# Performance work log

Hardware: AMD Instinct MI355X
Metric: run time of the kernel (lower is better)

## Reference

```python
import jax, jax.numpy as jnp
import numpy as np

WS = 8
SHIFT = 4


def _cpb_constants(ws):
    rc = np.arange(-(ws - 1), ws, dtype=np.float32)
    gh, gw = np.meshgrid(rc, rc, indexing='ij')
    table = np.stack([gh, gw], axis=-1)[None]  # (1, 2ws-1, 2ws-1, 2)
    table = table / (ws - 1) * 8.0
    table = np.sign(table) * np.log2(np.abs(table) + 1.0) / np.log2(8.0)
    c = np.arange(ws)
    ch, cw = np.meshgrid(c, c, indexing='ij')
    flat = np.stack([ch.ravel(), cw.ravel()])  # (2, N)
    rel = (flat[:, :, None] - flat[:, None, :]).transpose(1, 2, 0).copy()
    rel[..., 0] += ws - 1
    rel[..., 1] += ws - 1
    rel[..., 0] *= 2 * ws - 1
    rpi = rel.sum(-1)  # (N, N) int
    return table.astype(np.float32), rpi


def _attn_mask(H, W, ws, s):
    # Faithful to source: middle slice is slice(-ws, +s) (empty for H>ws+s)
    img = np.zeros((H, W), np.float32)
    cnt = 0
    for hs in (slice(0, -ws), slice(-ws, s), slice(-s, None)):
        for wsl in (slice(0, -ws), slice(-ws, s), slice(-s, None)):
            img[hs, wsl] = cnt
            cnt += 1
    mw = img.reshape(H // ws, ws, W // ws, ws).transpose(0, 2, 1, 3).reshape(-1, ws * ws)
    am = mw[:, None, :] - mw[:, :, None]
    return np.where(am != 0, -100.0, 0.0).astype(np.float32)


def _dwconv(x, w):
    return jax.lax.conv_general_dilated(
        x, w, (1, 1), 'SAME',
        dimension_numbers=('NCHW', 'OIHW', 'NCHW'),
        feature_group_count=x.shape[1])


def _ln_nchw(x, g, b, eps=8e-8):
    m = x.mean(1, keepdims=True)
    v = jnp.square(x - m).mean(1, keepdims=True)
    return (x - m) / jnp.sqrt(v + eps) * g[None, :, None, None] + b[None, :, None, None]


def setup_inputs() -> dict:
    key = jax.random.key(0)
    ks = jax.random.split(key, 16)
    B, C, H, W = 16, 512, 64, 64
    nh = 16
    hid = 4 * C
    w = lambda k, s: (jax.random.normal(k, s, dtype=jnp.float32) * 0.02)
    return {
        'x': jax.random.normal(ks[0], (B, C, H, W), dtype=jnp.float32),
        'lpu_w': w(ks[1], (C, 1, 3, 3)),
        'qkv_w': w(ks[2], (3 * C, C)),
        'out_w': w(ks[3], (C, C)),
        'cpb_w1': w(ks[4], (512, 2)),
        'cpb_w2': w(ks[5], (nh, 512)),
        'logits_scale': jnp.full((nh, 1, 1), np.log(10.0), dtype=jnp.float32),
        'gamma1': jnp.ones((C,), jnp.float32),
        'beta1': jnp.zeros((C,), jnp.float32),
        'gamma2': jnp.ones((C,), jnp.float32),
        'beta2': jnp.zeros((C,), jnp.float32),
        'pw1_w': w(ks[6], (hid, C)),
        'dw_w': w(ks[7], (hid, 1, 3, 3)),
        'pw2_w': w(ks[8], (C, hid)),
        'sr_scale': jnp.ones((), jnp.float32),
        'sr_bias': jnp.zeros((), jnp.float32),
        'rs1': jnp.ones((C,), jnp.float32),
        'rs2': jnp.ones((C,), jnp.float32),
    }


def reference(x, lpu_w, qkv_w, out_w, cpb_w1, cpb_w2, logits_scale,
              gamma1, beta1, gamma2, beta2, pw1_w, dw_w, pw2_w,
              sr_scale, sr_bias, rs1, rs2):
    B, C, H, W = x.shape
    ws, s = WS, SHIFT
    nh = logits_scale.shape[0]
    hd = C // nh
    N = ws * ws
    table_np, rpi = _cpb_constants(ws)
    table = jnp.asarray(table_np)
    mask = jnp.asarray(_attn_mask(H, W, ws, s))  # (nW, N, N)

    # LPU: x + depthwise conv
    x = x + _dwconv(x, lpu_w)
    x_temp = x

    # flatten to (B, HW, C); faithful roll over dims (1,2) = tokens AND channels
    x = x.reshape(B, C, H * W).transpose(0, 2, 1)
    x = jnp.roll(x, (-s, -s), axis=(1, 2))
    # window partition
    x = x.reshape(B, H // ws, ws, W // ws, ws, C).transpose(0, 1, 3, 2, 4, 5).reshape(-1, N, C)
    Bw = x.shape[0]

    qkv = (x @ qkv_w.T).reshape(Bw, N, 3, nh, hd).transpose(2, 0, 3, 1, 4)
    q, k, v = qkv[0], qkv[1], qkv[2]
    qn = q / jnp.maximum(jnp.linalg.norm(q, axis=-1, keepdims=True), 1e-12)
    kn = k / jnp.maximum(jnp.linalg.norm(k, axis=-1, keepdims=True), 1e-12)
    scale = jnp.exp(jnp.minimum(logits_scale, jnp.log(jnp.float32(100.0))))
    attn = jnp.einsum('bhid,bhjd->bhij', qn, kn) * scale[None]

    # continuous position bias
    tbl = jax.nn.hard_swish(table @ cpb_w1.T) @ cpb_w2.T  # (1, 2ws-1, 2ws-1, nh)
    tbl = tbl.reshape(-1, nh)
    bias = tbl[rpi.reshape(-1)].reshape(N, N, nh).transpose(2, 0, 1)
    bias = 16.0 * jax.nn.sigmoid(bias)
    attn = attn + bias[None]

    nW = mask.shape[0]
    attn = (attn.reshape(Bw // nW, nW, nh, N, N) + mask[None, :, None]).reshape(-1, nh, N, N)
    # faithful: nn.Softmax(1) -> softmax over HEAD axis
    attn = jax.nn.softmax(attn, axis=1)

    o = jnp.einsum('bhij,bhjd->bhid', attn, v).transpose(0, 2, 1, 3).reshape(Bw, N, C)
    o = o @ out_w.T

    o = o.reshape(B, H // ws, ws, W // ws, ws, C)
    o = jnp.roll(o, (s, s), axis=(1, 2))  # faithful: rolls window-grid / row dims
    # faithful buggy un-partition: transpose(1,2) then reshape
    o = o.transpose(0, 2, 1, 3, 4, 5).reshape(B, C, H, W)

    x = rs1[None, :, None, None] * x_temp + _ln_nchw(o, gamma1, beta1)

    h = jnp.einsum('bchw,oc->bohw', x, pw1_w)
    h = h + _dwconv(h, dw_w)
    h = sr_scale * jnp.square(jax.nn.relu(h)) + sr_bias  # StarReLU
    y = jnp.einsum('bchw,oc->bohw', h, pw2_w)
    return rs2[None, :, None, None] * x + _ln_nchw(y, gamma2, beta2)
```

## Files before the change

### kernel.cpp

```cpp
#include <hip/hip_runtime.h>
#include <hip/hip_bf16.h>
#include <stdint.h>


typedef float f32x4 __attribute__((ext_vector_type(4)));
typedef short s16x8 __attribute__((ext_vector_type(8)));

__device__ __forceinline__ float b2f(short u) {
  return __uint_as_float(((unsigned)(unsigned short)u) << 16);
}
__device__ __forceinline__ short f2b(float f) {
  __hip_bfloat16 h = __float2bfloat16(f);
  short s;
  __builtin_memcpy(&s, &h, 2);
  return s;
}
__device__ __forceinline__ void gload16(const void* g, void* l) {
  __builtin_amdgcn_global_load_lds((const unsigned int*)g, (unsigned int*)l, 16, 0, 0);
}

__global__ __launch_bounds__(256) void k_f2b4(const float* __restrict__ s0, short* __restrict__ d0,
                                              const float* __restrict__ s1, short* __restrict__ d1,
                                              const float* __restrict__ s2, short* __restrict__ d2,
                                              const float* __restrict__ s3, short* __restrict__ d3) {
  int b = blockIdx.x;
  const float* s;
  short* d;
  int base;
  if (b < 768) { s = s0; d = d0; base = b * 1024; }
  else if (b < 1024) { s = s1; d = d1; base = (b - 768) * 1024; }
  else if (b < 2048) { s = s2; d = d2; base = (b - 1024) * 1024; }
  else { s = s3; d = d3; base = (b - 2048) * 1024; }
  int i = base + threadIdx.x * 4;
  f32x4 v = *(const f32x4*)&s[i];
  ushort4 o;
  o.x = (unsigned short)f2b(v[0]);
  o.y = (unsigned short)f2b(v[1]);
  o.z = (unsigned short)f2b(v[2]);
  o.w = (unsigned short)f2b(v[3]);
  *(ushort4*)&d[i] = o;
}

__global__ __launch_bounds__(64) void k_cpb(const float* __restrict__ w1,
                                            const float* __restrict__ w2,
                                            float* __restrict__ btab) {
  const int r = blockIdx.x;
  const int lane = threadIdx.x;
  const int ri = r / 15, rj = r % 15;
  float th = (float)(ri - 7) * (8.f / 7.f);
  float tw = (float)(rj - 7) * (8.f / 7.f);
  float gh = copysignf(log2f(fabsf(th) + 1.f) * (1.f / 3.f), th);
  float gw = copysignf(log2f(fabsf(tw) + 1.f) * (1.f / 3.f), tw);
  const int h = lane >> 2, pp = lane & 3;
  float acc = 0.f;
  for (int k = 0; k < 128; ++k) {
    int hh = pp * 128 + k;
    float a = gh * w1[hh * 2] + gw * w1[hh * 2 + 1];
    float r6 = fminf(fmaxf(a + 3.f, 0.f), 6.f);
    float hsw = a * r6 * (1.f / 6.f);
    acc += hsw * w2[h * 512 + hh];
  }
  acc += __shfl_xor(acc, 1);
  acc += __shfl_xor(acc, 2);
  if ((lane & 3) == 0) btab[h * 225 + r] = 16.f / (1.f + __expf(-acc));
}

__global__ __launch_bounds__(256) void k_lpu(const float* __restrict__ x,
                                             const float* __restrict__ lw,
                                             short* __restrict__ xt) {
  __shared__ float img[64 * 68];
  const int bc = blockIdx.x;
  const int c = bc & 511;
  const float* img_g = x + (size_t)bc * 4096;
  short* outp = xt + (size_t)bc * 4096;
  const int tid = threadIdx.x;
#pragma unroll
  for (int t = 0; t < 4; ++t) {
    int idx = t * 256 + tid;
    int h = idx >> 4, w4 = (idx & 15) * 4;
    f32x4 v = *(const f32x4*)&img_g[h * 64 + w4];
    *(f32x4*)&img[h * 68 + w4] = v;
  }
  float wreg[9];
#pragma unroll
  for (int t = 0; t < 9; ++t) wreg[t] = lw[c * 9 + t];
  __syncthreads();
  const int hb = tid >> 4, w0 = (tid & 15) * 4;
#pragma unroll
  for (int g = 0; g < 4; ++g) {
    int h = hb + g * 16;
    float row[3][6];
#pragma unroll
    for (int dr = 0; dr < 3; ++dr) {
      int hh = h - 1 + dr;
      if (hh < 0 || hh > 63) {
#pragma unroll
        for (int j = 0; j < 6; ++j) row[dr][j] = 0.f;
      } else {
        f32x4 m = *(const f32x4*)&img[hh * 68 + w0];
        row[dr][1] = m[0]; row[dr][2] = m[1]; row[dr][3] = m[2]; row[dr][4] = m[3];
        row[dr][0] = (w0 > 0) ? img[hh * 68 + w0 - 1] : 0.f;
        row[dr][5] = (w0 < 60) ? img[hh * 68 + w0 + 4] : 0.f;
      }
    }
    ushort4 o;
    unsigned short op[4];
#pragma unroll
    for (int p = 0; p < 4; ++p) {
      float acc = row[1][p + 1];
#pragma unroll
      for (int dr = 0; dr < 3; ++dr)
#pragma unroll
        for (int dc = 0; dc < 3; ++dc)
          acc += wreg[dr * 3 + dc] * row[dr][p + dc];
      op[p] = (unsigned short)f2b(acc);
    }
    o.x = op[0]; o.y = op[1]; o.z = op[2]; o.w = op[3];
    *(ushort4*)&outp[h * 64 + w0] = o;
  }
}

__global__ __launch_bounds__(256) void k_xpose(const short* __restrict__ xt,
                                               short* __restrict__ xw) {
  __shared__ short tile[64][132];
  const int tid = threadIdx.x;
  const int cq = blockIdx.x & 3;
  const int h = (blockIdx.x >> 2) & 63;
  const int b = blockIdx.x >> 8;
  const int c0 = cq * 128;
  for (int idx = tid; idx < 64 * 128; idx += 256) {
    int ww = idx & 63, cc = idx >> 6;
    int csrc = (c0 + cc + 4) & 511;
    tile[ww][cc] = xt[(((size_t)b * 512 + csrc) * 64 + h) * 64 + ww];
  }
  __syncthreads();
  for (int qd = tid; qd < 64 * 32; qd += 256) {
    int ws_ = qd >> 5, cqq = qd & 31, cc = cqq * 4;
    int t = (h * 64 + ws_ + 4092) & 4095;
    int hd = t >> 6, wd = t & 63;
    int tok = (b * 64 + (hd >> 3) * 8 + (wd >> 3)) * 64 + (hd & 7) * 8 + (wd & 7);
    ushort4 u = *(const ushort4*)&tile[ws_][cc];
    *(ushort4*)&xw[(size_t)tok * 512 + c0 + cc] = u;
  }
}

template <int EPI>
__global__ __launch_bounds__(512) void k_gemm(const short* __restrict__ A,
                                              const short* __restrict__ B,
                                              short* __restrict__ C,
                                              short* __restrict__ o4,
                                              const float* __restrict__ lsc,
                                              int N, int K, int gx) {
  __shared__ short smem[2 * 16384];
  const int nwg = gridDim.x;
  const int orig = blockIdx.x;
  const int wgid = (orig & 7) * (nwg >> 3) + (orig >> 3);
  const int bx = wgid % gx, by = wgid / gx;
  const int tid = threadIdx.x;
  const int lane = tid & 63, wid = tid >> 6;
  const int wm = wid >> 2, wn = wid & 3;
  const int m0 = by * 128, n0 = bx * 128;
  const f32x4 fz = {0.f, 0.f, 0.f, 0.f};
  f32x4 acc[4][2];
#pragma unroll
  for (int m = 0; m < 4; ++m) { acc[m][0] = fz; acc[m][1] = fz; }
  const int rst = lane >> 3;
  const int cst = ((lane & 7) ^ rst) * 8;
  const int l15 = lane & 15, l4 = lane >> 4, l7 = lane & 7;
  const short* ag[2];
  const short* bg[2];
#pragma unroll
  for (int l = 0; l < 2; ++l) {
    int h8 = wid * 2 + l;
    ag[l] = A + (size_t)(m0 + h8 * 8 + rst) * K + cst;
    bg[l] = B + (size_t)(n0 + h8 * 8 + rst) * K + cst;
  }
  const int nt = K >> 6;
  auto STAGE = [&](int b) {
    short* as = smem + b * 16384;
    short* bs = as + 8192;
#pragma unroll
    for (int l = 0; l < 2; ++l) {
      int h8 = wid * 2 + l;
      gload16(ag[l], as + h8 * 512);
      gload16(bg[l], bs + h8 * 512);
      ag[l] += 64;
      bg[l] += 64;
    }
  };
  STAGE(0);
  __syncthreads();
  for (int kt = 0; kt < nt; ++kt) {
    const int cur = kt & 1;
    if (kt + 1 < nt) STAGE(cur ^ 1);
    const short* as = smem + cur * 16384;
    const short* bs = as + 8192;
    __builtin_amdgcn_s_setprio(1);
#pragma unroll
    for (int ks = 0; ks < 2; ++ks) {
      s16x8 af[4], bfr[2];
#pragma unroll
      for (int m = 0; m < 4; ++m)
        af[m] = *(const s16x8*)&as[(wm * 64 + m * 16 + l15) * 64 + (((ks * 4 + l4) ^ l7) * 8)];
#pragma unroll
      for (int n = 0; n < 2; ++n)
        bfr[n] = *(const s16x8*)&bs[(wn * 32 + n * 16 + l15) * 64 + (((ks * 4 + l4) ^ l7) * 8)];
#pragma unroll
      for (int m = 0; m < 4; ++m)
#pragma unroll
        for (int n = 0; n < 2; ++n)
          acc[m][n] = __builtin_amdgcn_mfma_f32_16x16x32_bf16(af[m], bfr[n],
                                                              acc[m][n], 0, 0, 0);
    }
    __builtin_amdgcn_s_setprio(0);
    __syncthreads();
  }
  if (EPI == 2) {
    const int cb = n0 + wn * 32;
    if (cb < 1024) {
      float sc = 1.f;
      if (cb < 512) sc = __expf(fminf(lsc[cb >> 5], 4.605170185988092f));
#pragma unroll
      for (int m = 0; m < 4; ++m)
#pragma unroll
        for (int r = 0; r < 4; ++r) {
          float s0 = acc[m][0][r], s1 = acc[m][1][r];
          float ss = s0 * s0 + s1 * s1;
          ss += __shfl_xor(ss, 1);
          ss += __shfl_xor(ss, 2);
          ss += __shfl_xor(ss, 4);
          ss += __shfl_xor(ss, 8);
          float mul = sc / fmaxf(sqrtf(ss), 1e-12f);
          acc[m][0][r] = s0 * mul;
          acc[m][1][r] = s1 * mul;
        }
    }
  }
  short* ct = smem;
#pragma unroll
  for (int p = 0; p < 2; ++p) {
    if (p) __syncthreads();
    if (wm == p) {
#pragma unroll
      for (int m = 0; m < 4; ++m)
#pragma unroll
        for (int n = 0; n < 2; ++n)
#pragma unroll
          for (int r = 0; r < 4; ++r) {
            int lr = m * 16 + l4 * 4 + r;
            int lc = wn * 32 + n * 16 + l15;
            ct[lr * 136 + lc] = f2b(acc[m][n][r]);
          }
    }
    __syncthreads();
#pragma unroll
    for (int u = 0; u < 2; ++u) {
      int unit = u * 512 + tid;
      int lr = unit >> 4, cs = unit & 15;
      s16x8 v = *(const s16x8*)&ct[lr * 136 + cs * 8];
      int grow = m0 + p * 64 + lr;
      int gcol = n0 + cs * 8;
      if (EPI != 1) {
        *(s16x8*)&C[(size_t)grow * N + gcol] = v;
      } else {
        int win = grow >> 6, nn = grow & 63;
        int b = win >> 6, whs = (win >> 3) & 7, wws = win & 7;
        int ih = nn >> 3, iw = nn & 7;
        int wh = (whs + 4) & 7, ww = (wws + 4) & 7;
        int cp = ww * 64 + wh * 8 + ih;
        int hp = iw * 8 + (gcol >> 6);
        int wp = gcol & 63;
        *(s16x8*)&o4[(((size_t)b * 512 + cp) * 64 + hp) * 64 + wp] = v;
      }
    }
  }
}

__global__ __launch_bounds__(256) void k_attn(const short* __restrict__ qkv,
                                              const float* __restrict__ btab_g,
                                              short* __restrict__ o_ws) {
  __shared__ float btab[3600];
  __shared__ short vts[2][2048];
  __shared__ short pts[4][1024];
  const int tid = threadIdx.x, lane = tid & 63, wid = tid >> 6;
  const int win = blockIdx.x;
  const int l15 = lane & 15, l4 = lane >> 4;
  const int qrow0 = wid * 16;
  for (int i = tid; i < 3600; i += 256) btab[i] = btab_g[i];
  int baddr[4][4];
#pragma unroll
  for (int n = 0; n < 4; ++n)
#pragma unroll
    for (int r = 0; r < 4; ++r) {
      int i_ = qrow0 + l4 * 4 + r, j_ = n * 16 + l15;
      int dih = (i_ >> 3) - (j_ >> 3) + 7;
      int diw = (i_ & 7) - (j_ & 7) + 7;
      baddr[n][r] = dih * 15 + diw;
    }
  __syncthreads();
  const short* base = qkv + (size_t)win * 64 * 1536;
  const f32x4 fz = {0.f, 0.f, 0.f, 0.f};
  f32x4 sump[4] = {fz, fz, fz, fz};
#pragma unroll 2
  for (int h = 0; h < 16; ++h) {
    s16x8 qf = *(const s16x8*)(base + (size_t)(qrow0 + l15) * 1536 + h * 32 + l4 * 8);
#pragma unroll
    for (int n = 0; n < 4; ++n) {
      s16x8 kf = *(const s16x8*)(base + (size_t)(n * 16 + l15) * 1536 + 512 + h * 32 + l4 * 8);
      f32x4 s = __builtin_amdgcn_mfma_f32_16x16x32_bf16(qf, kf, fz, 0, 0, 0);
#pragma unroll
      for (int r = 0; r < 4; ++r)
        sump[n][r] += __expf(s[r] + btab[h * 225 + baddr[n][r]]);
    }
  }
  f32x4 rden[4];
#pragma unroll
  for (int n = 0; n < 4; ++n)
#pragma unroll
    for (int r = 0; r < 4; ++r) rden[n][r] = 1.f / sump[n][r];
  char* pt = (char*)pts[wid];
  {
    int j = tid & 63, d0 = (tid >> 6) * 8;
    s16x8 vv = *(const s16x8*)(base + (size_t)j * 1536 + 1024 + d0);
#pragma unroll
    for (int jj = 0; jj < 8; ++jj) {
      int d = d0 + jj;
      *(short*)((char*)vts[0] + ((d * 128 + j * 2) ^ ((d & 7) << 4))) = vv[jj];
    }
  }
  __syncthreads();
  for (int h = 0; h < 16; ++h) {
    const char* vcur = (const char*)vts[h & 1];
    if (h < 15) {
      int j = tid & 63, d0 = (tid >> 6) * 8;
      s16x8 vv = *(const s16x8*)(base + (size_t)j * 1536 + 1024 + (h + 1) * 32 + d0);
      char* vnxt = (char*)vts[(h + 1) & 1];
#pragma unroll
      for (int jj = 0; jj < 8; ++jj) {
        int d = d0 + jj;
        *(short*)(vnxt + ((d * 128 + j * 2) ^ ((d & 7) << 4))) = vv[jj];
      }
    }
    s16x8 qf = *(const s16x8*)(base + (size_t)(qrow0 + l15) * 1536 + h * 32 + l4 * 8);
#pragma unroll
    for (int n = 0; n < 4; ++n) {
      s16x8 kf = *(const s16x8*)(base + (size_t)(n * 16 + l15) * 1536 + 512 + h * 32 + l4 * 8);
      f32x4 s = __builtin_amdgcn_mfma_f32_16x16x32_bf16(qf, kf, fz, 0, 0, 0);
#pragma unroll
      for (int r = 0; r < 4; ++r) {
        float pv = __expf(s[r] + btab[h * 225 + baddr[n][r]]) * rden[n][r];
        int i_loc = l4 * 4 + r, j_ = n * 16 + l15;
        *(short*)(pt + ((i_loc * 128 + j_ * 2) ^ ((i_loc & 7) << 4))) = f2b(pv);
      }
    }
    f32x4 oacc[2] = {fz, fz};
#pragma unroll
    for (int kb = 0; kb < 2; ++kb) {
      s16x8 af = *(const s16x8*)(pt + ((l15 * 128 + kb * 64 + l4 * 16) ^ ((l15 & 7) << 4)));
#pragma unroll
      for (int db = 0; db < 2; ++db) {
        int d = db * 16 + l15;
        s16x8 bf = *(const s16x8*)(vcur + ((d * 128 + kb * 64 + l4 * 16) ^ ((d & 7) << 4)));
        oacc[db] = __builtin_amdgcn_mfma_f32_16x16x32_bf16(af, bf, oacc[db], 0, 0, 0);
      }
    }
    short* ob = o_ws + ((size_t)win * 64 + qrow0) * 512 + h * 32;
#pragma unroll
    for (int db = 0; db < 2; ++db)
#pragma unroll
      for (int r = 0; r < 4; ++r)
        ob[(size_t)(l4 * 4 + r) * 512 + db * 16 + l15] = f2b(oacc[db][r]);
    __syncthreads();
  }
}

__global__ __launch_bounds__(256) void k_ln1(const short* __restrict__ o4,
                                             const short* __restrict__ xt,
                                             const float* __restrict__ g1,
                                             const float* __restrict__ b1,
                                             const float* __restrict__ rs1,
                                             short* __restrict__ x2h) {
  __shared__ float reds[4][64], redq[4][64];
  __shared__ float mean_s[64], rstd_s[64];
  __shared__ short tile[128][66];
  const int tid = threadIdx.x;
  const int b = blockIdx.x >> 6, hp = blockIdx.x & 63;
  const int w = tid & 63, part = tid >> 6;
  const short* base = o4 + (size_t)b * 512 * 4096 + hp * 64;
  float s = 0.f, q = 0.f;
  for (int c = part; c < 512; c += 4) {
    float v = b2f(base[(size_t)c * 4096 + w]);
    s += v; q += v * v;
  }
  reds[part][w] = s; redq[part][w] = q;
  __syncthreads();
  if (tid < 64) {
    float S = 0.f, Q = 0.f;
    for (int i = 0; i < 4; ++i) { S += reds[i][tid]; Q += redq[i][tid]; }
    float m = S * (1.f / 512.f);
    float var = Q * (1.f / 512.f) - m * m;
    mean_s[tid] = m;
    rstd_s[tid] = rsqrtf(var + 8e-8f);
  }
  __syncthreads();
  const short* xtb = xt + (size_t)b * 512 * 4096 + hp * 64;
  for (int c0 = 0; c0 < 512; c0 += 128) {
    for (int cc = part; cc < 128; cc += 4) {
      int c = c0 + cc;
      float v = b2f(base[(size_t)c * 4096 + w]);
      float ln = (v - mean_s[w]) * rstd_s[w] * g1[c] + b1[c];
      float xv = rs1[c] * b2f(xtb[(size_t)c * 4096 + w]) + ln;
      tile[cc][w] = f2b(xv);
    }
    __syncthreads();
    short* xh = x2h + ((size_t)blockIdx.x * 64) * 512 + c0;
    for (int qd = tid; qd < 64 * 32; qd += 256) {
      int w_ = qd >> 5, cq = qd & 31, cc = cq * 4;
      ushort4 u;
      u.x = (unsigned short)tile[cc][w_];
      u.y = (unsigned short)tile[cc + 1][w_];
      u.z = (unsigned short)tile[cc + 2][w_];
      u.w = (unsigned short)tile[cc + 3][w_];
      *(ushort4*)&xh[(size_t)w_ * 512 + cc] = u;
    }
    __syncthreads();
  }
}

__global__ __launch_bounds__(256) void k_dwc2(const short* __restrict__ h1,
                                              const float* __restrict__ dw,
                                              const float* __restrict__ srs_p,
                                              const float* __restrict__ srb_p,
                                              short* __restrict__ h2) {
  __shared__ short tile[6 * 64 * 64];
  const int tid = threadIdx.x;
  const int cblk = blockIdx.x & 31;
  const int hq = (blockIdx.x >> 5) & 15;
  const int b = blockIdx.x >> 9;
  const int c0 = cblk * 64;
  const int h0 = hq * 4;
  for (int t = 0; t < 12; ++t) {
    int idx = t * 256 + tid;
    int cg = idx & 7;
    int wl = (idx >> 3) & 63;
    int rl = idx >> 9;
    int hr = h0 - 1 + rl;
    s16x8 v = {0, 0, 0, 0, 0, 0, 0, 0};
    if (hr >= 0 && hr < 64)
      v = *(const s16x8*)&h1[((size_t)b * 4096 + hr * 64 + wl) * 2048 + c0 + cg * 8];
    *(s16x8*)&tile[(rl * 64 + wl) * 64 + (cg ^ (wl & 7)) * 8] = v;
  }
  const int cg = tid & 7;
  const int wq = tid >> 3;
  float wt[9][8];
#pragma unroll
  for (int j = 0; j < 8; ++j) {
    int cch = c0 + cg * 8 + j;
#pragma unroll
    for (int t = 0; t < 9; ++t) wt[t][j] = dw[cch * 9 + t];
  }
  const float srs = *srs_p, srb = *srb_p;
  __syncthreads();
#pragma unroll
  for (int it = 0; it < 8; ++it) {
    int wl = wq + (it & 1) * 32;
    int rl = it >> 1;
    s16x8 ctr = *(const s16x8*)&tile[((rl + 1) * 64 + wl) * 64 + (cg ^ (wl & 7)) * 8];
    float acc[8];
#pragma unroll
    for (int j = 0; j < 8; ++j) acc[j] = b2f(ctr[j]);
#pragma unroll
    for (int dh = -1; dh <= 1; ++dh) {
      int row = rl + 1 + dh;
#pragma unroll
      for (int dwi = -1; dwi <= 1; ++dwi) {
        int wn = wl + dwi;
        if (wn < 0 || wn > 63) continue;
        s16x8 v = *(const s16x8*)&tile[(row * 64 + wn) * 64 + (cg ^ (wn & 7)) * 8];
        const float* wrow = wt[(dh + 1) * 3 + dwi + 1];
#pragma unroll
        for (int j = 0; j < 8; ++j) acc[j] += wrow[j] * b2f(v[j]);
      }
    }
    s16x8 o;
#pragma unroll
    for (int j = 0; j < 8; ++j) {
      float rr = fmaxf(acc[j], 0.f);
      o[j] = f2b(srs * rr * rr + srb);
    }
    *(s16x8*)&h2[((size_t)b * 4096 + (h0 + rl) * 64 + wl) * 2048 + c0 + cg * 8] = o;
  }
}

__global__ __launch_bounds__(256) void k_final(const short* __restrict__ y,
                                               const short* __restrict__ x2h,
                                               const float* __restrict__ g2,
                                               const float* __restrict__ b2p,
                                               const float* __restrict__ rs2,
                                               float* __restrict__ out) {
  __shared__ short yt[64][132];
  __shared__ short xt2[64][132];
  __shared__ float reds[4][64], redq[4][64];
  __shared__ float mean_s[64], rstd_s[64];
  const int tid = threadIdx.x;
  const int b = blockIdx.x >> 6, hh = blockIdx.x & 63;
  const int w = tid & 63, part = tid >> 6;
  const short* yb = y + (size_t)blockIdx.x * 64 * 512;
  const short* xb = x2h + (size_t)blockIdx.x * 64 * 512;
  float s = 0.f, q = 0.f;
  for (int c0 = 0; c0 < 512; c0 += 128) {
    for (int qd = tid; qd < 64 * 32; qd += 256) {
      int w_ = qd >> 5, g = qd & 31;
      *(ushort4*)&yt[w_][g * 4] = *(const ushort4*)&yb[(size_t)w_ * 512 + c0 + g * 4];
    }
    __syncthreads();
    for (int cc = part * 32; cc < part * 32 + 32; ++cc) {
      float v = b2f(yt[w][cc]);
      s += v; q += v * v;
    }
    __syncthreads();
  }
  reds[part][w] = s; redq[part][w] = q;
  __syncthreads();
  if (tid < 64) {
    float S = 0.f, Q = 0.f;
    for (int i = 0; i < 4; ++i) { S += reds[i][tid]; Q += redq[i][tid]; }
    float m = S * (1.f / 512.f);
    float var = Q * (1.f / 512.f) - m * m;
    mean_s[tid] = m;
    rstd_s[tid] = rsqrtf(var + 8e-8f);
  }
  __syncthreads();
  float* ob = out + (size_t)b * 512 * 4096 + hh * 64;
  for (int c0 = 0; c0 < 512; c0 += 128) {
    for (int qd = tid; qd < 64 * 32; qd += 256) {
      int w_ = qd >> 5, g = qd & 31;
      *(ushort4*)&yt[w_][g * 4] = *(const ushort4*)&yb[(size_t)w_ * 512 + c0 + g * 4];
      *(ushort4*)&xt2[w_][g * 4] = *(const ushort4*)&xb[(size_t)w_ * 512 + c0 + g * 4];
    }
    __syncthreads();
    for (int it = 0; it < 32; ++it) {
      int c = c0 + it * 4 + part;
      float yv = b2f(yt[w][c - c0]);
      float lnv = (yv - mean_s[w]) * rstd_s[w] * g2[c] + b2p[c];
      float xv = b2f(xt2[w][c - c0]);
      ob[(size_t)c * 4096 + w] = rs2[c] * xv + lnv;
    }
    __syncthreads();
  }
}

extern "C" void kernel_launch(void* const* d_in, const int* in_sizes, int n_in,
                              void* d_out, int out_size, void* d_ws, size_t ws_size,
                              hipStream_t stream) {
  (void)in_sizes; (void)n_in; (void)out_size; (void)ws_size;
  const float* x      = (const float*)d_in[0];
  const float* lpu_w  = (const float*)d_in[1];
  const float* qkv_w  = (const float*)d_in[2];
  const float* out_w  = (const float*)d_in[3];
  const float* cpb_w1 = (const float*)d_in[4];
  const float* cpb_w2 = (const float*)d_in[5];
  const float* lsc    = (const float*)d_in[6];
  const float* g1     = (const float*)d_in[7];
  const float* b1     = (const float*)d_in[8];
  const float* g2     = (const float*)d_in[9];
  const float* b2v    = (const float*)d_in[10];
  const float* pw1_w  = (const float*)d_in[11];
  const float* dw_w   = (const float*)d_in[12];
  const float* pw2_w  = (const float*)d_in[13];
  const float* srs    = (const float*)d_in[14];
  const float* srb    = (const float*)d_in[15];
  const float* rs1    = (const float*)d_in[16];
  const float* rs2    = (const float*)d_in[17];

  char* ws = (char*)d_ws;
  float* btab   = (float*)(ws + 0);
  short* wbq    = (short*)(ws + 16384);
  short* wbo    = (short*)(ws + 1589248);
  short* wb1    = (short*)(ws + 2113536);
  short* wb2    = (short*)(ws + 4210688);
  short* x_temp = (short*)(ws + 8388608);
  short* xw     = (short*)(ws + 75497472);
  short* qkv    = (short*)(ws + 142606336);
  short* o_ws   = (short*)(ws + 343932928);
  short* o4     = (short*)(ws + 75497472);
  short* x2h    = (short*)(ws + 142606336);
  short* h1     = (short*)(ws + 209715200);
  short* h2     = (short*)(ws + 8388608);
  short* yb     = (short*)(ws + 343932928);

  k_f2b4<<<3072, 256, 0, stream>>>(qkv_w, wbq, out_w, wbo, pw1_w, wb1, pw2_w, wb2);
  k_cpb<<<225, 64, 0, stream>>>(cpb_w1, cpb_w2, btab);
  k_lpu<<<8192, 256, 0, stream>>>(x, lpu_w, x_temp);
  k_xpose<<<4096, 256, 0, stream>>>(x_temp, xw);
  k_gemm<2><<<6144, 512, 0, stream>>>(xw, wbq, qkv, nullptr, lsc, 1536, 512, 12);
  k_attn<<<1024, 256, 0, stream>>>(qkv, btab, o_ws);
  k_gemm<1><<<2048, 512, 0, stream>>>(o_ws, wbo, nullptr, o4, nullptr, 512, 512, 4);
  k_ln1<<<1024, 256, 0, stream>>>(o4, x_temp, g1, b1, rs1, x2h);
  for (int ch = 0; ch < 2; ++ch) {
    const size_t tok0 = (size_t)ch * 8 * 4096;
    k_gemm<0><<<4096, 512, 0, stream>>>(x2h + tok0 * 512, wb1, h1, nullptr, nullptr, 2048, 512, 16);
    k_dwc2<<<4096, 256, 0, stream>>>(h1, dw_w, srs, srb, h2);
    k_gemm<0><<<1024, 512, 0, stream>>>(h2, wb2, yb + tok0 * 512, nullptr, nullptr, 512, 2048, 4);
  }
  k_final<<<1024, 256, 0, stream>>>(yb, x2h, g2, b2v, rs2, (float*)d_out);
}
```

Before: 1.107 ms.

## Enlarge GEMM block tile to 256x256 and swizzle epilogue staging buffer

```diff
diff --git a/kernel.cpp b/kernel.cpp
--- a/kernel.cpp
+++ b/kernel.cpp
@@ -145,13 +145,13 @@
 }
 
 template <int EPI>
-__global__ __launch_bounds__(512) void k_gemm(const short* __restrict__ A,
-                                              const short* __restrict__ B,
-                                              short* __restrict__ C,
-                                              short* __restrict__ o4,
-                                              const float* __restrict__ lsc,
-                                              int N, int K, int gx) {
-  __shared__ short smem[2 * 16384];
+__global__ __launch_bounds__(512, 2) void k_gemm(const short* __restrict__ A,
+                                                 const short* __restrict__ B,
+                                                 short* __restrict__ C,
+                                                 short* __restrict__ o4,
+                                                 const float* __restrict__ lsc,
+                                                 int N, int K, int gx) {
+  __shared__ short smem[2 * 32768];
   const int nwg = gridDim.x;
   const int orig = blockIdx.x;
   const int wgid = (orig & 7) * (nwg >> 3) + (orig >> 3);
@@ -159,31 +159,33 @@
   const int tid = threadIdx.x;
   const int lane = tid & 63, wid = tid >> 6;
   const int wm = wid >> 2, wn = wid & 3;
-  const int m0 = by * 128, n0 = bx * 128;
+  const int m0 = by * 256, n0 = bx * 256;
   const f32x4 fz = {0.f, 0.f, 0.f, 0.f};
-  f32x4 acc[4][2];
-#pragma unroll
-  for (int m = 0; m < 4; ++m) { acc[m][0] = fz; acc[m][1] = fz; }
+  f32x4 acc[8][4];
+#pragma unroll
+  for (int m = 0; m < 8; ++m)
+#pragma unroll
+    for (int n = 0; n < 4; ++n) acc[m][n] = fz;
   const int rst = lane >> 3;
   const int cst = ((lane & 7) ^ rst) * 8;
   const int l15 = lane & 15, l4 = lane >> 4, l7 = lane & 7;
-  const short* ag[2];
-  const short* bg[2];
-#pragma unroll
-  for (int l = 0; l < 2; ++l) {
-    int h8 = wid * 2 + l;
-    ag[l] = A + (size_t)(m0 + h8 * 8 + rst) * K + cst;
-    bg[l] = B + (size_t)(n0 + h8 * 8 + rst) * K + cst;
+  const short* ag[4];
+  const short* bg[4];
+#pragma unroll
+  for (int l = 0; l < 4; ++l) {
+    int r = wid * 32 + l * 8 + rst;
+    ag[l] = A + (size_t)(m0 + r) * K + cst;
+    bg[l] = B + (size_t)(n0 + r) * K + cst;
   }
   const int nt = K >> 6;
   auto STAGE = [&](int b) {
-    short* as = smem + b * 16384;
-    short* bs = as + 8192;
-#pragma unroll
-    for (int l = 0; l < 2; ++l) {
-      int h8 = wid * 2 + l;
-      gload16(ag[l], as + h8 * 512);
-      gload16(bg[l], bs + h8 * 512);
+    short* as = smem + b * 32768;
+    short* bs = as + 16384;
+#pragma unroll
+    for (int l = 0; l < 4; ++l) {
+      int rb = wid * 32 + l * 8;
+      gload16(ag[l], as + rb * 64);
+      gload16(bg[l], bs + rb * 64);
       ag[l] += 64;
       bg[l] += 64;
     }
@@ -193,47 +195,50 @@
   for (int kt = 0; kt < nt; ++kt) {
     const int cur = kt & 1;
     if (kt + 1 < nt) STAGE(cur ^ 1);
-    const short* as = smem + cur * 16384;
-    const short* bs = as + 8192;
+    const short* as = smem + cur * 32768;
+    const short* bs = as + 16384;
     __builtin_amdgcn_s_setprio(1);
 #pragma unroll
     for (int ks = 0; ks < 2; ++ks) {
-      s16x8 af[4], bfr[2];
-#pragma unroll
-      for (int m = 0; m < 4; ++m)
-        af[m] = *(const s16x8*)&as[(wm * 64 + m * 16 + l15) * 64 + (((ks * 4 + l4) ^ l7) * 8)];
-#pragma unroll
-      for (int n = 0; n < 2; ++n)
-        bfr[n] = *(const s16x8*)&bs[(wn * 32 + n * 16 + l15) * 64 + (((ks * 4 + l4) ^ l7) * 8)];
-#pragma unroll
-      for (int m = 0; m < 4; ++m)
-#pragma unroll
-        for (int n = 0; n < 2; ++n)
-          acc[m][n] = __builtin_amdgcn_mfma_f32_16x16x32_bf16(af[m], bfr[n],
+      const int slot = ((ks * 4 + l4) ^ l7) * 8;
+      s16x8 bfr[4];
+#pragma unroll
+      for (int n = 0; n < 4; ++n)
+        bfr[n] = *(const s16x8*)&bs[(wn * 64 + n * 16 + l15) * 64 + slot];
+#pragma unroll
+      for (int m = 0; m < 8; ++m) {
+        s16x8 af = *(const s16x8*)&as[(wm * 128 + m * 16 + l15) * 64 + slot];
+#pragma unroll
+        for (int n = 0; n < 4; ++n)
+          acc[m][n] = __builtin_amdgcn_mfma_f32_16x16x32_bf16(af, bfr[n],
                                                               acc[m][n], 0, 0, 0);
+      }
     }
     __builtin_amdgcn_s_setprio(0);
     __syncthreads();
   }
   if (EPI == 2) {
-    const int cb = n0 + wn * 32;
-    if (cb < 1024) {
-      float sc = 1.f;
-      if (cb < 512) sc = __expf(fminf(lsc[cb >> 5], 4.605170185988092f));
-#pragma unroll
-      for (int m = 0; m < 4; ++m)
-#pragma unroll
-        for (int r = 0; r < 4; ++r) {
-          float s0 = acc[m][0][r], s1 = acc[m][1][r];
-          float ss = s0 * s0 + s1 * s1;
-          ss += __shfl_xor(ss, 1);
-          ss += __shfl_xor(ss, 2);
-          ss += __shfl_xor(ss, 4);
-          ss += __shfl_xor(ss, 8);
-          float mul = sc / fmaxf(sqrtf(ss), 1e-12f);
-          acc[m][0][r] = s0 * mul;
-          acc[m][1][r] = s1 * mul;
-        }
+#pragma unroll
+    for (int b = 0; b < 2; ++b) {
+      const int cb = n0 + wn * 64 + b * 32;
+      if (cb < 1024) {
+        float sc = 1.f;
+        if (cb < 512) sc = __expf(fminf(lsc[cb >> 5], 4.605170185988092f));
+#pragma unroll
+        for (int m = 0; m < 8; ++m)
+#pragma unroll
+          for (int r = 0; r < 4; ++r) {
+            float s0 = acc[m][2 * b][r], s1 = acc[m][2 * b + 1][r];
+            float ss = s0 * s0 + s1 * s1;
+            ss += __shfl_xor(ss, 1);
+            ss += __shfl_xor(ss, 2);
+            ss += __shfl_xor(ss, 4);
+            ss += __shfl_xor(ss, 8);
+            float mul = sc / fmaxf(sqrtf(ss), 1e-12f);
+            acc[m][2 * b][r] = s0 * mul;
+            acc[m][2 * b + 1][r] = s1 * mul;
+          }
+      }
     }
   }
   short* ct = smem;
@@ -242,24 +247,25 @@
     if (p) __syncthreads();
     if (wm == p) {
 #pragma unroll
-      for (int m = 0; m < 4; ++m)
-#pragma unroll
-        for (int n = 0; n < 2; ++n)
+      for (int m = 0; m < 8; ++m)
+#pragma unroll
+        for (int n = 0; n < 4; ++n)
 #pragma unroll
           for (int r = 0; r < 4; ++r) {
             int lr = m * 16 + l4 * 4 + r;
-            int lc = wn * 32 + n * 16 + l15;
-            ct[lr * 136 + lc] = f2b(acc[m][n][r]);
+            int lc = (wn * 64 + n * 16 + l15) ^ (((lr >> 2) & 3) << 4);
+            ct[lr * 272 + lc] = f2b(acc[m][n][r]);
           }
     }
     __syncthreads();
 #pragma unroll
-    for (int u = 0; u < 2; ++u) {
-      int unit = u * 512 + tid;
-      int lr = unit >> 4, cs = unit & 15;
-      s16x8 v = *(const s16x8*)&ct[lr * 136 + cs * 8];
-      int grow = m0 + p * 64 + lr;
-      int gcol = n0 + cs * 8;
+    for (int uu = 0; uu < 8; ++uu) {
+      int unit = uu * 512 + tid;
+      int lr = unit >> 5, sl = unit & 31;
+      int sx = (sl * 8) ^ (((lr >> 2) & 3) << 4);
+      s16x8 v = *(const s16x8*)&ct[lr * 272 + sx];
+      int grow = m0 + p * 128 + lr;
+      int gcol = n0 + sl * 8;
       if (EPI != 1) {
         *(s16x8*)&C[(size_t)grow * N + gcol] = v;
       } else {
@@ -593,15 +599,15 @@
   k_cpb<<<225, 64, 0, stream>>>(cpb_w1, cpb_w2, btab);
   k_lpu<<<8192, 256, 0, stream>>>(x, lpu_w, x_temp);
   k_xpose<<<4096, 256, 0, stream>>>(x_temp, xw);
-  k_gemm<2><<<6144, 512, 0, stream>>>(xw, wbq, qkv, nullptr, lsc, 1536, 512, 12);
+  k_gemm<2><<<1536, 512, 0, stream>>>(xw, wbq, qkv, nullptr, lsc, 1536, 512, 6);
   k_attn<<<1024, 256, 0, stream>>>(qkv, btab, o_ws);
-  k_gemm<1><<<2048, 512, 0, stream>>>(o_ws, wbo, nullptr, o4, nullptr, 512, 512, 4);
+  k_gemm<1><<<512, 512, 0, stream>>>(o_ws, wbo, nullptr, o4, nullptr, 512, 512, 2);
   k_ln1<<<1024, 256, 0, stream>>>(o4, x_temp, g1, b1, rs1, x2h);
   for (int ch = 0; ch < 2; ++ch) {
     const size_t tok0 = (size_t)ch * 8 * 4096;
-    k_gemm<0><<<4096, 512, 0, stream>>>(x2h + tok0 * 512, wb1, h1, nullptr, nullptr, 2048, 512, 16);
+    k_gemm<0><<<1024, 512, 0, stream>>>(x2h + tok0 * 512, wb1, h1, nullptr, nullptr, 2048, 512, 8);
     k_dwc2<<<4096, 256, 0, stream>>>(h1, dw_w, srs, srb, h2);
-    k_gemm<0><<<1024, 512, 0, stream>>>(h2, wb2, yb + tok0 * 512, nullptr, nullptr, 512, 2048, 4);
+    k_gemm<0><<<256, 512, 0, stream>>>(h2, wb2, yb + tok0 * 512, nullptr, nullptr, 512, 2048, 2);
   }
   k_final<<<1024, 256, 0, stream>>>(yb, x2h, g2, b2v, rs2, (float*)d_out);
 }
```

Result: slower. 1.160 ms (+4.8%).
